# Kernel optimization log

Hardware: AMD Instinct MI355X
Metric: run time of the kernel (lower is better)

Reference implementation:

```python
import jax, jax.numpy as jnp
import numpy as np

H, W = 480, 640
ICP_W = 10.0
N_ITER = 20
FTOL = 1e-3
XTOL = 1e-8
DIST_THR = 200.0 / 15.0
NORMAL_THR = 0.94


def _skew(w):
    z = jnp.zeros((), w.dtype)
    return jnp.stack([
        jnp.stack([z, -w[2], w[1]]),
        jnp.stack([w[2], z, -w[0]]),
        jnp.stack([-w[1], w[0], z]),
    ])


def _exp_se3(xi):
    # xi = (v, w); SE3 exponential map (lie_se3_to_SE3)
    v, w = xi[:3], xi[3:]
    th2 = jnp.sum(w * w)
    th = jnp.sqrt(th2)
    small = th < 1e-8
    ths = jnp.where(small, 1.0, th)
    A = jnp.where(small, 1.0 - th2 / 6.0, jnp.sin(ths) / ths)
    B = jnp.where(small, 0.5 - th2 / 24.0, (1.0 - jnp.cos(ths)) / (ths * ths))
    C = jnp.where(small, 1.0 / 6.0 - th2 / 120.0, (ths - jnp.sin(ths)) / (ths * ths * ths))
    Wx = _skew(w)
    W2 = Wx @ Wx
    R = jnp.eye(3, dtype=xi.dtype) + A * Wx + B * W2
    V = jnp.eye(3, dtype=xi.dtype) + B * Wx + C * W2
    t = V @ v
    T = jnp.eye(4, dtype=xi.dtype)
    T = T.at[:3, :3].set(R).at[:3, 3].set(t)
    return T


def _bilinear(img, u, v):
    # img [H,W]; u,v [N] float pixel coords
    u0 = jnp.floor(u)
    v0 = jnp.floor(v)
    du = u - u0
    dv = v - v0
    u0i = jnp.clip(u0.astype(jnp.int32), 0, W - 1)
    u1i = jnp.clip(u0i + 1, 0, W - 1)
    v0i = jnp.clip(v0.astype(jnp.int32), 0, H - 1)
    v1i = jnp.clip(v0i + 1, 0, H - 1)
    I00 = img[v0i, u0i]; I01 = img[v0i, u1i]
    I10 = img[v1i, u0i]; I11 = img[v1i, u1i]
    return (I00 * (1 - du) + I01 * du) * (1 - dv) + (I10 * (1 - du) + I11 * du) * dv


def _forward(depth_ref, normals_ref, gray_ref, gray_target, points_target, normals_target, intrinsics):
    dt = depth_ref.dtype
    fx, fy = intrinsics[0, 0], intrinsics[1, 1]
    cx, cy = intrinsics[0, 2], intrinsics[1, 2]
    vv, uu = jnp.meshgrid(jnp.arange(H, dtype=dt), jnp.arange(W, dtype=dt), indexing='ij')
    Z = depth_ref
    # ref PointCloud.from_depth: backprojection [N,3]
    P = jnp.stack([(uu - cx) / fx * Z, (vv - cy) / fy * Z, Z], -1).reshape(-1, 3)
    Nr = normals_ref.reshape(-1, 3)
    Ir = gray_ref.reshape(-1)
    gy_img, gx_img = jnp.gradient(gray_target)  # d/dv, d/du
    Nflt = jnp.asarray(H * W, dt)

    def step(carry, _):
        x, conv, cost = carry
        T = _exp_se3(x)
        R, t = T[:3, :3], T[:3, 3]
        Pt = P @ R.T + t  # transformed ref points [N,3]
        Zt = Pt[:, 2]
        okz = Zt > 1e-6
        Zs = jnp.where(okz, Zt, 1.0)
        u = fx * Pt[:, 0] / Zs + cx
        v = fy * Pt[:, 1] / Zs + cy
        inb = okz & (u >= 0) & (u <= W - 1) & (v >= 0) & (v <= H - 1)
        ui = jnp.clip(jnp.round(u).astype(jnp.int32), 0, W - 1)
        vi = jnp.clip(jnp.round(v).astype(jnp.int32), 0, H - 1)
        # --- ICP point-to-plane, projective association ---
        q = points_target[vi, ui]    # [N,3]
        nq = normals_target[vi, ui]  # [N,3]
        d = Pt - q
        nref_rot = Nr @ R.T
        valid_icp = inb & (jnp.sum(d * d, -1) < DIST_THR ** 2) & (jnp.sum(nref_rot * nq, -1) > NORMAL_THR)
        m_icp = valid_icp.astype(dt)
        r_icp = jnp.sum(nq * d, -1) * m_icp                              # [N]
        J_icp = jnp.concatenate([nq, jnp.cross(Pt, nq)], -1) * m_icp[:, None]  # [N,6]
        # --- RGB photometric ---
        m_rgb = inb.astype(dt)
        It = _bilinear(gray_target, u, v)
        r_rgb = (It - Ir) * m_rgb
        gxs = _bilinear(gx_img, u, v)
        gys = _bilinear(gy_img, u, v)
        # grad_I * d(projection)/d(point)
        gp = jnp.stack([
            gxs * fx / Zs,
            gys * fy / Zs,
            -(gxs * fx * Pt[:, 0] + gys * fy * Pt[:, 1]) / (Zs * Zs),
        ], -1)
        J_rgb = jnp.concatenate([gp, jnp.cross(Pt, gp)], -1) * m_rgb[:, None]
        # --- normal equations ---
        A = ICP_W * (J_icp.T @ J_icp) + J_rgb.T @ J_rgb
        b = ICP_W * (J_icp.T @ r_icp) + J_rgb.T @ r_rgb
        x0 = jnp.linalg.solve(A + 1e-9 * jnp.eye(6, dtype=dt), b)
        new_cost = ICP_W * jnp.sum(r_icp ** 2) / Nflt + jnp.sum(r_rgb ** 2) / Nflt
        c = conv | (new_cost < FTOL) | (jnp.linalg.norm(x0) < XTOL * (XTOL + jnp.linalg.norm(x)))
        x_new = jnp.where(c, x, x - x0)
        cost_new = jnp.where(conv, cost, new_cost)
        return (x_new, c, cost_new), None

    init = (jnp.zeros(6, dt), jnp.array(False), jnp.asarray(0.0, dt))
    (x, conv, cost), _ = jax.lax.scan(step, init, None, length=N_ITER)
    return _exp_se3(x), cost


def setup_inputs() -> dict:
    key = jax.random.key(0)
    ks = jax.random.split(key, 6)
    intrinsics = jnp.array([[525.0, 0.0, 319.5], [0.0, 525.0, 239.5], [0.0, 0.0, 1.0]], jnp.float32)
    fx, fy, cx, cy = 525.0, 525.0, 319.5, 239.5
    depth_ref = 0.5 + 1.5 * jax.random.uniform(ks[0], (H, W), jnp.float32)
    depth_t = 0.5 + 1.5 * jax.random.uniform(ks[1], (H, W), jnp.float32)
    vv, uu = jnp.meshgrid(jnp.arange(H, dtype=jnp.float32), jnp.arange(W, dtype=jnp.float32), indexing='ij')
    points_target = jnp.stack([(uu - cx) / fx * depth_t, (vv - cy) / fy * depth_t, depth_t], -1)
    def mk_normals(k):
        n = 0.1 * jax.random.normal(k, (H, W, 3), jnp.float32) + jnp.array([0.0, 0.0, -1.0])
        return n / jnp.linalg.norm(n, axis=-1, keepdims=True)
    normals_ref = mk_normals(ks[2])
    normals_target = mk_normals(ks[3])
    gray_ref = jax.random.uniform(ks[4], (H, W), jnp.float32)
    gray_target = jax.random.uniform(ks[5], (H, W), jnp.float32)
    return {
        'depth_ref': depth_ref,
        'normals_ref': normals_ref,
        'gray_ref': gray_ref,
        'gray_target': gray_target,
        'points_target': points_target,
        'normals_target': normals_target,
        'intrinsics': intrinsics,
    }


def reference(depth_ref, normals_ref, gray_ref, gray_target, points_target, normals_target, intrinsics):
    return _forward(depth_ref, normals_ref, gray_ref, gray_target, points_target, normals_target, intrinsics)
```

## Files before the change

kernel.cpp:

```cpp
#include <hip/hip_runtime.h>
#include <math.h>

#define HH 480
#define WW 640
#define NPIX (HH*WW)
#define NACC 29
#define TPB 256
#define PXPT 3
#define MB 400
#define NLEAF 16
#define GSZ (MB/NLEAF)

#define WS_PKT 64
#define WS_P0 512
#define WS_P1 (WS_P0 + NACC*MB)
#define WS_G4 23808
#define WS_NR (WS_G4 + NPIX*4)
#define WS_PZ (WS_NR + NPIX*4)
#define WS_BIG_END (WS_PZ + NPIX*4)

__device__ __forceinline__ int ld_i_sc1(const int* p) {
    return __hip_atomic_load(p, __ATOMIC_RELAXED, __HIP_MEMORY_SCOPE_AGENT);
}
__device__ __forceinline__ float ld_f_sc1(const float* p) {
    return __hip_atomic_load(p, __ATOMIC_RELAXED, __HIP_MEMORY_SCOPE_AGENT);
}
__device__ __forceinline__ void st_f_sc1(float* p, float v) {
    __hip_atomic_store(p, v, __ATOMIC_RELAXED, __HIP_MEMORY_SCOPE_AGENT);
}
__device__ __forceinline__ void arrive(int* bar, int bid) {
    int* lc = bar + 128 + 16 * (bid & (NLEAF - 1));
    int a = __hip_atomic_fetch_add(lc, 1, __ATOMIC_RELAXED, __HIP_MEMORY_SCOPE_AGENT);
    if (((a + 1) % GSZ) == 0)
        __hip_atomic_fetch_add(bar + 16, 1, __ATOMIC_RELAXED, __HIP_MEMORY_SCOPE_AGENT);
}

__device__ __forceinline__ float gradu(const float* g, int v, int u) {
    const float* row = g + v * WW;
    if (u == 0)      return row[1] - row[0];
    if (u == WW - 1) return row[WW - 1] - row[WW - 2];
    return 0.5f * (row[u + 1] - row[u - 1]);
}
__device__ __forceinline__ float gradv(const float* g, int v, int u) {
    if (v == 0)      return g[WW + u] - g[u];
    if (v == HH - 1) return g[(HH - 1) * WW + u] - g[(HH - 2) * WW + u];
    return 0.5f * (g[(v + 1) * WW + u] - g[(v - 1) * WW + u]);
}

__device__ void exp_se3_f32(const float* xi, float* T) {
    float v0 = xi[0], v1 = xi[1], v2 = xi[2];
    float w0 = xi[3], w1 = xi[4], w2 = xi[5];
    float th2 = w0 * w0 + w1 * w1 + w2 * w2;
    float th = sqrtf(th2);
    bool small = th < 1e-8f;
    float ths = small ? 1.0f : th;
    float A = small ? (1.0f - th2 / 6.0f) : (sinf(ths) / ths);
    float B = small ? (0.5f - th2 / 24.0f) : ((1.0f - cosf(ths)) / (ths * ths));
    float C = small ? (1.0f / 6.0f - th2 / 120.0f) : ((ths - sinf(ths)) / (ths * ths * ths));
    float Wx[9] = { 0.f, -w2,  w1,
                    w2,  0.f, -w0,
                   -w1,  w0,  0.f };
    float W2[9];
    #pragma unroll
    for (int i = 0; i < 3; i++)
        #pragma unroll
        for (int j = 0; j < 3; j++) {
            float s = 0.f;
            #pragma unroll
            for (int k = 0; k < 3; k++) s += Wx[i * 3 + k] * Wx[k * 3 + j];
            W2[i * 3 + j] = s;
        }
    float R[9], V[9];
    #pragma unroll
    for (int i = 0; i < 9; i++) {
        float id = (i == 0 || i == 4 || i == 8) ? 1.0f : 0.0f;
        R[i] = id + A * Wx[i] + B * W2[i];
        V[i] = id + B * Wx[i] + C * W2[i];
    }
    float t0 = V[0] * v0 + V[1] * v1 + V[2] * v2;
    float t1 = V[3] * v0 + V[4] * v1 + V[5] * v2;
    float t2 = V[6] * v0 + V[7] * v1 + V[8] * v2;
    T[0] = R[0]; T[1] = R[1]; T[2]  = R[2]; T[3]  = t0;
    T[4] = R[3]; T[5] = R[4]; T[6]  = R[5]; T[7]  = t1;
    T[8] = R[6]; T[9] = R[7]; T[10] = R[8]; T[11] = t2;
    T[12] = 0.f; T[13] = 0.f; T[14] = 0.f; T[15] = 1.f;
}

__device__ __forceinline__ void accum_point(float* acc, const float* J, float r, float w, int costslot) {
    int k = 0;
    #pragma unroll
    for (int i = 0; i < 6; i++) {
        #pragma unroll
        for (int j = i; j < 6; j++) { acc[k] += w * (J[i] * J[j]); k++; }
        acc[21 + i] += w * (J[i] * r);
    }
    acc[costslot] += r * r;
}

template <int PACKED>
__global__ __launch_bounds__(TPB, 2) void fused_icp(
    const float* __restrict__ depth_ref,
    const float* __restrict__ normals_ref,
    const float* __restrict__ gray_ref,
    const float* __restrict__ gray_target,
    const float* __restrict__ points_target,
    const float* __restrict__ normals_target,
    const float* __restrict__ K,
    float* __restrict__ ws,
    float* __restrict__ out)
{
    const int tid = threadIdx.x;
    const int bid = blockIdx.x;
    const float fx = K[0], cx = K[2], fy = K[4], cy = K[5];
    int* bar = (int*)ws;
    float* pkt = ws + WS_PKT;
    int sync_no = 0;
    float4* g4  = (float4*)(ws + WS_G4);
    float4* nr4 = (float4*)(ws + WS_NR);
    float4* pz4 = (float4*)(ws + WS_PZ);

    if (PACKED) {
        int base = bid * (TPB * PXPT) + tid;
        #pragma unroll
        for (int k = 0; k < PXPT; k++) {
            int p = base + k * TPB;
            int v = p / WW, u = p - v * WW;
            float4 c;
            c.x = gray_target[p];
            c.y = gradu(gray_target, v, u);
            c.z = gradv(gray_target, v, u);
            c.w = 0.f;
            g4[p] = c;
            float4 n;
            n.x = normals_ref[3 * p];
            n.y = normals_ref[3 * p + 1];
            n.z = normals_ref[3 * p + 2];
            n.w = depth_ref[p];
            nr4[p] = n;
            float4 z;
            z.x = points_target[3 * p + 2];
            z.y = normals_target[3 * p];
            z.z = normals_target[3 * p + 1];
            z.w = normals_target[3 * p + 2];
            pz4[p] = z;
        }
        __threadfence();
        __syncthreads();
        if (tid == 0) arrive(bar, bid);
        sync_no++;
        if (bid == 0 && tid == 0) {
            while (ld_i_sc1(bar + 16) < NLEAF * sync_no) __builtin_amdgcn_s_sleep(1);
            asm volatile("s_waitcnt vmcnt(0)" ::: "memory");
            __hip_atomic_store(bar, sync_no, __ATOMIC_RELAXED, __HIP_MEMORY_SCOPE_AGENT);
        }
        if (tid == 0) {
            while (ld_i_sc1(bar) < sync_no) __builtin_amdgcn_s_sleep(4);
        }
        __syncthreads();
    }

    __shared__ float spose[12];
    __shared__ float sx[6];
    __shared__ float sconv, scost;
    __shared__ float lds[4][NACC];
    __shared__ double part8[NACC * 8];
    __shared__ double sums[NACC];

    if (tid == 0) {
        spose[0] = 1.f; spose[1] = 0.f; spose[2] = 0.f;
        spose[3] = 0.f; spose[4] = 1.f; spose[5] = 0.f;
        spose[6] = 0.f; spose[7] = 0.f; spose[8] = 1.f;
        spose[9] = 0.f; spose[10] = 0.f; spose[11] = 0.f;
        #pragma unroll
        for (int i = 0; i < 6; i++) sx[i] = 0.f;
        sconv = 0.f; scost = 0.f;
    }
    __syncthreads();

    for (int it = 0; it < 20; ++it) {
        const float R00 = spose[0], R01 = spose[1], R02 = spose[2];
        const float R10 = spose[3], R11 = spose[4], R12 = spose[5];
        const float R20 = spose[6], R21 = spose[7], R22 = spose[8];
        const float t0 = spose[9], t1 = spose[10], t2 = spose[11];

        float acc[NACC];
        #pragma unroll
        for (int i = 0; i < NACC; i++) acc[i] = 0.f;

        int pbase = bid * (TPB * PXPT) + tid;
        #pragma unroll
        for (int kk = 0; kk < PXPT; kk++) {
            int p = pbase + kk * TPB;
            int vv = p / WW;
            int uu = p - vv * WW;

            float nr0, nr1, nr2, Z;
            if (PACKED) {
                float4 n = nr4[p];
                nr0 = n.x; nr1 = n.y; nr2 = n.z; Z = n.w;
            } else {
                Z = depth_ref[p];
                nr0 = normals_ref[3 * p]; nr1 = normals_ref[3 * p + 1]; nr2 = normals_ref[3 * p + 2];
            }
            float Px = ((float)uu - cx) / fx * Z;
            float Py = ((float)vv - cy) / fy * Z;
            float Pz = Z;
            float Ptx = R00 * Px + R01 * Py + R02 * Pz + t0;
            float Pty = R10 * Px + R11 * Py + R12 * Pz + t1;
            float Ptz = R20 * Px + R21 * Py + R22 * Pz + t2;
            bool okz = Ptz > 1e-6f;
            float Zs = okz ? Ptz : 1.0f;
            float u = fx * Ptx / Zs + cx;
            float v = fy * Pty / Zs + cy;
            bool inb = okz && (u >= 0.f) && (u <= (float)(WW - 1)) && (v >= 0.f) && (v <= (float)(HH - 1));
            if (!inb) continue;

            int ui = (int)rintf(u); ui = ui < 0 ? 0 : (ui > WW - 1 ? WW - 1 : ui);
            int vi = (int)rintf(v); vi = vi < 0 ? 0 : (vi > HH - 1 ? HH - 1 : vi);
            int ti = vi * WW + ui;
            float qx, qy, qz, nqx, nqy, nqz;
            if (PACKED) {
                float4 z = pz4[ti];
                qz = z.x; nqx = z.y; nqy = z.z; nqz = z.w;
                qx = (((float)ui) - cx) / fx * qz;
                qy = (((float)vi) - cy) / fy * qz;
            } else {
                qx = points_target[3 * ti]; qy = points_target[3 * ti + 1]; qz = points_target[3 * ti + 2];
                nqx = normals_target[3 * ti]; nqy = normals_target[3 * ti + 1]; nqz = normals_target[3 * ti + 2];
            }
            float dx = Ptx - qx, dy = Pty - qy, dz = Ptz - qz;
            float nrx = R00 * nr0 + R01 * nr1 + R02 * nr2;
            float nry = R10 * nr0 + R11 * nr1 + R12 * nr2;
            float nrz = R20 * nr0 + R21 * nr1 + R22 * nr2;
            const float DIST2 = (float)((200.0 / 15.0) * (200.0 / 15.0));
            if ((dx * dx + dy * dy + dz * dz) < DIST2 &&
                (nrx * nqx + nry * nqy + nrz * nqz) > 0.94f) {
                float r = nqx * dx + nqy * dy + nqz * dz;
                float J[6] = { nqx, nqy, nqz,
                               Pty * nqz - Ptz * nqy,
                               Ptz * nqx - Ptx * nqz,
                               Ptx * nqy - Pty * nqx };
                accum_point(acc, J, r, 10.0f, 27);
            }
            float u0f = floorf(u), v0f = floorf(v);
            float du = u - u0f, dv = v - v0f;
            int u0 = (int)u0f; u0 = u0 < 0 ? 0 : (u0 > WW - 1 ? WW - 1 : u0);
            int u1 = (u0 + 1 > WW - 1) ? WW - 1 : u0 + 1;
            int v0 = (int)v0f; v0 = v0 < 0 ? 0 : (v0 > HH - 1 ? HH - 1 : v0);
            int v1 = (v0 + 1 > HH - 1) ? HH - 1 : v0 + 1;
            int i00 = v0 * WW + u0, i01 = v0 * WW + u1, i10 = v1 * WW + u0, i11 = v1 * WW + u1;
            float I00, I01, I10, I11, gx00, gx01, gx10, gx11, gy00, gy01, gy10, gy11;
            if (PACKED) {
                float4 c00 = g4[i00], c01 = g4[i01], c10 = g4[i10], c11 = g4[i11];
                I00 = c00.x; gx00 = c00.y; gy00 = c00.z;
                I01 = c01.x; gx01 = c01.y; gy01 = c01.z;
                I10 = c10.x; gx10 = c10.y; gy10 = c10.z;
                I11 = c11.x; gx11 = c11.y; gy11 = c11.z;
            } else {
                const float* g = gray_target;
                I00 = g[i00]; I01 = g[i01]; I10 = g[i10]; I11 = g[i11];
                gx00 = gradu(g, v0, u0); gx01 = gradu(g, v0, u1);
                gx10 = gradu(g, v1, u0); gx11 = gradu(g, v1, u1);
                gy00 = gradv(g, v0, u0); gy01 = gradv(g, v0, u1);
                gy10 = gradv(g, v1, u0); gy11 = gradv(g, v1, u1);
            }
            float It  = (I00 * (1.f - du) + I01 * du) * (1.f - dv) + (I10 * (1.f - du) + I11 * du) * dv;
            float gxs = (gx00 * (1.f - du) + gx01 * du) * (1.f - dv) + (gx10 * (1.f - du) + gx11 * du) * dv;
            float gys = (gy00 * (1.f - du) + gy01 * du) * (1.f - dv) + (gy10 * (1.f - du) + gy11 * du) * dv;
            float rr = It - gray_ref[p];
            float gpx = gxs * fx / Zs;
            float gpy = gys * fy / Zs;
            float gpz = -(gxs * fx * Ptx + gys * fy * Pty) / (Zs * Zs);
            float J[6] = { gpx, gpy, gpz,
                           Pty * gpz - Ptz * gpy,
                           Ptz * gpx - Ptx * gpz,
                           Ptx * gpy - Pty * gpx };
            accum_point(acc, J, rr, 1.0f, 28);
        }

        #pragma unroll
        for (int q = 0; q < NACC; q++) {
            float vq = acc[q];
            #pragma unroll
            for (int off = 32; off >= 1; off >>= 1) vq += __shfl_xor(vq, off);
            acc[q] = vq;
        }
        int wave = tid >> 6;
        int lane = tid & 63;
        __syncthreads();
        if (lane == 0) {
            #pragma unroll
            for (int q = 0; q < NACC; q++) lds[wave][q] = acc[q];
        }
        __syncthreads();
        float* pbuf = ws + ((it & 1) ? WS_P1 : WS_P0);
        if (tid < NACC) {
            int q = tid;
            float s = lds[0][q] + lds[1][q] + lds[2][q] + lds[3][q];
            st_f_sc1(&pbuf[q * MB + bid], s);
        }
        __syncthreads();
        if (tid == 0) arrive(bar, bid);
        sync_no++;

        if (bid == 0) {
            if (tid == 0) {
                while (ld_i_sc1(bar + 16) < NLEAF * sync_no) __builtin_amdgcn_s_sleep(1);
            }
            __syncthreads();
            if (tid < NACC * 8) {
                int q = tid >> 3, s = tid & 7;
                const int CH = MB / 8;
                int lo = s * CH, hi = lo + CH;
                float* row = pbuf + q * MB;
                double a0 = 0, a1 = 0, a2 = 0, a3 = 0, a4 = 0, a5 = 0, a6 = 0, a7 = 0;
                int i = lo;
                for (; i + 8 <= hi; i += 8) {
                    a0 += (double)ld_f_sc1(&row[i]);
                    a1 += (double)ld_f_sc1(&row[i + 1]);
                    a2 += (double)ld_f_sc1(&row[i + 2]);
                    a3 += (double)ld_f_sc1(&row[i + 3]);
                    a4 += (double)ld_f_sc1(&row[i + 4]);
                    a5 += (double)ld_f_sc1(&row[i + 5]);
                    a6 += (double)ld_f_sc1(&row[i + 6]);
                    a7 += (double)ld_f_sc1(&row[i + 7]);
                }
                for (; i < hi; i++) a0 += (double)ld_f_sc1(&row[i]);
                part8[tid] = (((a0 + a1) + (a2 + a3)) + ((a4 + a5) + (a6 + a7)));
            }
            __syncthreads();
            if (tid < NACC) {
                double sm = 0.0;
                #pragma unroll
                for (int s = 0; s < 8; s++) sm += part8[tid * 8 + s];
                sums[tid] = sm;
            }
            __syncthreads();
            if (tid == 0) {
                double M[6][7];
                int k = 0;
                for (int i = 0; i < 6; i++)
                    for (int j = i; j < 6; j++) { M[i][j] = sums[k]; M[j][i] = sums[k]; k++; }
                for (int i = 0; i < 6; i++) { M[i][6] = sums[21 + i]; M[i][i] += 1e-9; }
                double new_cost = 10.0 * sums[27] / (double)NPIX + sums[28] / (double)NPIX;

                for (int c = 0; c < 6; c++) {
                    int piv = c; double mx = fabs(M[c][c]);
                    for (int r2 = c + 1; r2 < 6; r2++) {
                        double a = fabs(M[r2][c]);
                        if (a > mx) { mx = a; piv = r2; }
                    }
                    if (piv != c)
                        for (int j2 = 0; j2 < 7; j2++) { double tmp = M[c][j2]; M[c][j2] = M[piv][j2]; M[piv][j2] = tmp; }
                    double inv = 1.0 / M[c][c];
                    for (int r2 = c + 1; r2 < 6; r2++) {
                        double f = M[r2][c] * inv;
                        for (int j2 = c; j2 < 7; j2++) M[r2][j2] -= f * M[c][j2];
                    }
                }
                double x0[6];
                for (int i = 5; i >= 0; i--) {
                    double s = M[i][6];
                    for (int j = i + 1; j < 6; j++) s -= M[i][j] * x0[j];
                    x0[i] = s / M[i][i];
                }

                double nx0 = 0.0, nx = 0.0;
                float xf[6];
                for (int i = 0; i < 6; i++) {
                    xf[i] = sx[i];
                    nx0 += x0[i] * x0[i];
                    nx  += (double)xf[i] * (double)xf[i];
                }
                nx0 = sqrt(nx0); nx = sqrt(nx);
                bool convold = (sconv != 0.f);
                bool c2 = convold || (new_cost < 1e-3) || (nx0 < 1e-8 * (1e-8 + nx));
                float xn[6];
                for (int i = 0; i < 6; i++)
                    xn[i] = c2 ? xf[i] : (float)((double)xf[i] - x0[i]);
                for (int i = 0; i < 6; i++) sx[i] = xn[i];
                sconv = c2 ? 1.f : 0.f;
                if (!convold) scost = (float)new_cost;

                float T[16];
                exp_se3_f32(xn, T);
                st_f_sc1(&pkt[0], T[0]);  st_f_sc1(&pkt[1], T[1]);  st_f_sc1(&pkt[2], T[2]);
                st_f_sc1(&pkt[3], T[4]);  st_f_sc1(&pkt[4], T[5]);  st_f_sc1(&pkt[5], T[6]);
                st_f_sc1(&pkt[6], T[8]);  st_f_sc1(&pkt[7], T[9]);  st_f_sc1(&pkt[8], T[10]);
                st_f_sc1(&pkt[9], T[3]);  st_f_sc1(&pkt[10], T[7]); st_f_sc1(&pkt[11], T[11]);
                if (it == 19) {
                    for (int i = 0; i < 16; i++) out[i] = T[i];
                    out[16] = scost;
                }
                asm volatile("s_waitcnt vmcnt(0)" ::: "memory");
                __hip_atomic_store(bar, sync_no, __ATOMIC_RELAXED, __HIP_MEMORY_SCOPE_AGENT);
            }
        }

        if (tid == 0) {
            while (ld_i_sc1(bar) < sync_no) __builtin_amdgcn_s_sleep(4);
            asm volatile("" ::: "memory");
            #pragma unroll
            for (int i = 0; i < 12; i++) spose[i] = ld_f_sc1(&pkt[i]);
        }
        __syncthreads();
    }
}

extern "C" void kernel_launch(void* const* d_in, const int* in_sizes, int n_in,
                              void* d_out, int out_size, void* d_ws, size_t ws_size,
                              hipStream_t stream) {
    const float* depth_ref      = (const float*)d_in[0];
    const float* normals_ref    = (const float*)d_in[1];
    const float* gray_ref       = (const float*)d_in[2];
    const float* gray_target    = (const float*)d_in[3];
    const float* points_target  = (const float*)d_in[4];
    const float* normals_target = (const float*)d_in[5];
    const float* K              = (const float*)d_in[6];
    float* ws  = (float*)d_ws;
    float* out = (float*)d_out;

    hipMemsetAsync(d_ws, 0, 2048, stream);

    bool big = ws_size >= (size_t)WS_BIG_END * sizeof(float);
    if (big) {
        hipLaunchKernelGGL((fused_icp<1>), dim3(MB), dim3(TPB), 0, stream,
                           depth_ref, normals_ref, gray_ref, gray_target,
                           points_target, normals_target, K, ws, out);
    } else {
        hipLaunchKernelGGL((fused_icp<0>), dim3(MB), dim3(TPB), 0, stream,
                           depth_ref, normals_ref, gray_ref, gray_target,
                           points_target, normals_target, K, ws, out);
    }
}
```

Before: 538.3 us.

## Use 1024 persistent blocks with hierarchical leaf reduction and per-leaf release flags

Raises the persistent grid from 400 to 1024 blocks, each handling 300 pixels, and allows 4 blocks per CU through launch bounds. Blocks are remapped so each XCD group lands in its own leaf. The last block to arrive in each leaf pre-reduces that leaf's partials in double and publishes them, so block 0 only sums 16 leaf results. The single release flag becomes 16 per-leaf flags to spread out polling. The aim is to cut per-iteration grid-barrier and reduction latency. In exchange there are more blocks to synchronize and less pixel work per thread, and co-residency of all 1024 blocks is required to avoid deadlock.

```diff
diff --git a/kernel.cpp b/kernel.cpp
--- a/kernel.cpp
+++ b/kernel.cpp
@@ -6,15 +6,16 @@
 #define NPIX (HH*WW)
 #define NACC 29
 #define TPB 256
-#define PXPT 3
-#define MB 400
+#define NBLK 1024
+#define PPB 300
 #define NLEAF 16
-#define GSZ (MB/NLEAF)
-
-#define WS_PKT 64
-#define WS_P0 512
-#define WS_P1 (WS_P0 + NACC*MB)
-#define WS_G4 23808
+#define LSZ (NBLK/NLEAF)
+#define PB NBLK
+
+#define WS_PKT 400
+#define WS_LP 1024
+#define WS_P0 2048
+#define WS_G4 32768
 #define WS_NR (WS_G4 + NPIX*4)
 #define WS_PZ (WS_NR + NPIX*4)
 #define WS_BIG_END (WS_PZ + NPIX*4)
@@ -28,11 +29,11 @@
 __device__ __forceinline__ void st_f_sc1(float* p, float v) {
     __hip_atomic_store(p, v, __ATOMIC_RELAXED, __HIP_MEMORY_SCOPE_AGENT);
 }
-__device__ __forceinline__ void arrive(int* bar, int bid) {
-    int* lc = bar + 128 + 16 * (bid & (NLEAF - 1));
-    int a = __hip_atomic_fetch_add(lc, 1, __ATOMIC_RELAXED, __HIP_MEMORY_SCOPE_AGENT);
-    if (((a + 1) % GSZ) == 0)
-        __hip_atomic_fetch_add(bar + 16, 1, __ATOMIC_RELAXED, __HIP_MEMORY_SCOPE_AGENT);
+__device__ __forceinline__ double ld_d_sc1(const double* p) {
+    return __hip_atomic_load(p, __ATOMIC_RELAXED, __HIP_MEMORY_SCOPE_AGENT);
+}
+__device__ __forceinline__ void st_d_sc1(double* p, double v) {
+    __hip_atomic_store(p, v, __ATOMIC_RELAXED, __HIP_MEMORY_SCOPE_AGENT);
 }
 
 __device__ __forceinline__ float gradu(const float* g, int v, int u) {
@@ -98,7 +99,7 @@
 }
 
 template <int PACKED>
-__global__ __launch_bounds__(TPB, 2) void fused_icp(
+__global__ __launch_bounds__(TPB, 4) void fused_icp(
     const float* __restrict__ depth_ref,
     const float* __restrict__ normals_ref,
     const float* __restrict__ gray_ref,
@@ -110,20 +111,42 @@
     float* __restrict__ out)
 {
     const int tid = threadIdx.x;
-    const int bid = blockIdx.x;
+    const int wid = (blockIdx.x & 7) * (NBLK / 8) + (blockIdx.x >> 3);
+    const int leaf = wid / LSZ;
     const float fx = K[0], cx = K[2], fy = K[4], cy = K[5];
     int* bar = (int*)ws;
     float* pkt = ws + WS_PKT;
+    double* lp = (double*)(ws + WS_LP);
+    float* pbuf = ws + WS_P0;
     int sync_no = 0;
     float4* g4  = (float4*)(ws + WS_G4);
     float4* nr4 = (float4*)(ws + WS_NR);
     float4* pz4 = (float4*)(ws + WS_PZ);
 
+    __shared__ float spose[12];
+    __shared__ float sx[6];
+    __shared__ float sconv, scost;
+    __shared__ float lds[4][NACC];
+    __shared__ double part8[NACC * 8];
+    __shared__ double sums[NACC];
+    __shared__ int scloser;
+
+    if (tid == 0) {
+        spose[0] = 1.f; spose[1] = 0.f; spose[2] = 0.f;
+        spose[3] = 0.f; spose[4] = 1.f; spose[5] = 0.f;
+        spose[6] = 0.f; spose[7] = 0.f; spose[8] = 1.f;
+        spose[9] = 0.f; spose[10] = 0.f; spose[11] = 0.f;
+        #pragma unroll
+        for (int i = 0; i < 6; i++) sx[i] = 0.f;
+        sconv = 0.f; scost = 0.f;
+    }
+
     if (PACKED) {
-        int base = bid * (TPB * PXPT) + tid;
-        #pragma unroll
-        for (int k = 0; k < PXPT; k++) {
-            int p = base + k * TPB;
+        int base = wid * PPB;
+        for (int k = 0; k < 2; k++) {
+            int off = k * TPB + tid;
+            if (off >= PPB) break;
+            int p = base + off;
             int v = p / WW, u = p - v * WW;
             float4 c;
             c.x = gray_target[p];
@@ -145,37 +168,28 @@
             pz4[p] = z;
         }
         __threadfence();
-        __syncthreads();
-        if (tid == 0) arrive(bar, bid);
         sync_no++;
-        if (bid == 0 && tid == 0) {
+        __syncthreads();
+        if (tid == 0) {
+            int a = __hip_atomic_fetch_add(bar + 128 + 16 * leaf, 1, __ATOMIC_RELAXED, __HIP_MEMORY_SCOPE_AGENT);
+            scloser = ((a + 1) == LSZ * sync_no) ? 1 : 0;
+        }
+        __syncthreads();
+        if (scloser && tid == 0)
+            __hip_atomic_fetch_add(bar + 16, 1, __ATOMIC_RELAXED, __HIP_MEMORY_SCOPE_AGENT);
+        if (wid == 0 && tid == 0) {
             while (ld_i_sc1(bar + 16) < NLEAF * sync_no) __builtin_amdgcn_s_sleep(1);
             asm volatile("s_waitcnt vmcnt(0)" ::: "memory");
-            __hip_atomic_store(bar, sync_no, __ATOMIC_RELAXED, __HIP_MEMORY_SCOPE_AGENT);
+            for (int i = 0; i < NLEAF; i++)
+                __hip_atomic_store(bar + 512 + 16 * i, sync_no, __ATOMIC_RELAXED, __HIP_MEMORY_SCOPE_AGENT);
         }
         if (tid == 0) {
-            while (ld_i_sc1(bar) < sync_no) __builtin_amdgcn_s_sleep(4);
-        }
-        __syncthreads();
-    }
-
-    __shared__ float spose[12];
-    __shared__ float sx[6];
-    __shared__ float sconv, scost;
-    __shared__ float lds[4][NACC];
-    __shared__ double part8[NACC * 8];
-    __shared__ double sums[NACC];
-
-    if (tid == 0) {
-        spose[0] = 1.f; spose[1] = 0.f; spose[2] = 0.f;
-        spose[3] = 0.f; spose[4] = 1.f; spose[5] = 0.f;
-        spose[6] = 0.f; spose[7] = 0.f; spose[8] = 1.f;
-        spose[9] = 0.f; spose[10] = 0.f; spose[11] = 0.f;
-        #pragma unroll
-        for (int i = 0; i < 6; i++) sx[i] = 0.f;
-        sconv = 0.f; scost = 0.f;
-    }
-    __syncthreads();
+            while (ld_i_sc1(bar + 512 + 16 * leaf) < sync_no) __builtin_amdgcn_s_sleep(2);
+        }
+        __syncthreads();
+    } else {
+        __syncthreads();
+    }
 
     for (int it = 0; it < 20; ++it) {
         const float R00 = spose[0], R01 = spose[1], R02 = spose[2];
@@ -187,10 +201,12 @@
         #pragma unroll
         for (int i = 0; i < NACC; i++) acc[i] = 0.f;
 
-        int pbase = bid * (TPB * PXPT) + tid;
-        #pragma unroll
-        for (int kk = 0; kk < PXPT; kk++) {
-            int p = pbase + kk * TPB;
+        int base = wid * PPB;
+        #pragma unroll
+        for (int kk = 0; kk < 2; kk++) {
+            int off = kk * TPB + tid;
+            if (off >= PPB) break;
+            int p = base + off;
             int vv = p / WW;
             int uu = p - vv * WW;
 
@@ -293,40 +309,47 @@
             for (int q = 0; q < NACC; q++) lds[wave][q] = acc[q];
         }
         __syncthreads();
-        float* pbuf = ws + ((it & 1) ? WS_P1 : WS_P0);
         if (tid < NACC) {
             int q = tid;
             float s = lds[0][q] + lds[1][q] + lds[2][q] + lds[3][q];
-            st_f_sc1(&pbuf[q * MB + bid], s);
-        }
-        __syncthreads();
-        if (tid == 0) arrive(bar, bid);
+            st_f_sc1(&pbuf[q * PB + wid], s);
+        }
         sync_no++;
-
-        if (bid == 0) {
+        __syncthreads();
+        if (tid == 0) {
+            int a = __hip_atomic_fetch_add(bar + 128 + 16 * leaf, 1, __ATOMIC_RELAXED, __HIP_MEMORY_SCOPE_AGENT);
+            scloser = ((a + 1) == LSZ * sync_no) ? 1 : 0;
+        }
+        __syncthreads();
+        if (scloser) {
+            if (tid < NACC * 8) {
+                int q = tid >> 3, s = tid & 7;
+                const float* row = pbuf + q * PB + leaf * LSZ + s * 8;
+                double a0 = 0.0;
+                #pragma unroll
+                for (int j = 0; j < 8; j++) a0 += (double)ld_f_sc1(&row[j]);
+                part8[tid] = a0;
+            }
+            __syncthreads();
+            if (tid < NACC) {
+                double sm = 0.0;
+                #pragma unroll
+                for (int s = 0; s < 8; s++) sm += part8[tid * 8 + s];
+                st_d_sc1(&lp[tid * NLEAF + leaf], sm);
+            }
+            __syncthreads();
+            if (tid == 0)
+                __hip_atomic_fetch_add(bar + 16, 1, __ATOMIC_RELAXED, __HIP_MEMORY_SCOPE_AGENT);
+        }
+
+        if (wid == 0) {
             if (tid == 0) {
                 while (ld_i_sc1(bar + 16) < NLEAF * sync_no) __builtin_amdgcn_s_sleep(1);
             }
             __syncthreads();
             if (tid < NACC * 8) {
                 int q = tid >> 3, s = tid & 7;
-                const int CH = MB / 8;
-                int lo = s * CH, hi = lo + CH;
-                float* row = pbuf + q * MB;
-                double a0 = 0, a1 = 0, a2 = 0, a3 = 0, a4 = 0, a5 = 0, a6 = 0, a7 = 0;
-                int i = lo;
-                for (; i + 8 <= hi; i += 8) {
-                    a0 += (double)ld_f_sc1(&row[i]);
-                    a1 += (double)ld_f_sc1(&row[i + 1]);
-                    a2 += (double)ld_f_sc1(&row[i + 2]);
-                    a3 += (double)ld_f_sc1(&row[i + 3]);
-                    a4 += (double)ld_f_sc1(&row[i + 4]);
-                    a5 += (double)ld_f_sc1(&row[i + 5]);
-                    a6 += (double)ld_f_sc1(&row[i + 6]);
-                    a7 += (double)ld_f_sc1(&row[i + 7]);
-                }
-                for (; i < hi; i++) a0 += (double)ld_f_sc1(&row[i]);
-                part8[tid] = (((a0 + a1) + (a2 + a3)) + ((a4 + a5) + (a6 + a7)));
+                part8[tid] = ld_d_sc1(&lp[q * NLEAF + 2 * s]) + ld_d_sc1(&lp[q * NLEAF + 2 * s + 1]);
             }
             __syncthreads();
             if (tid < NACC) {
@@ -393,12 +416,13 @@
                     out[16] = scost;
                 }
                 asm volatile("s_waitcnt vmcnt(0)" ::: "memory");
-                __hip_atomic_store(bar, sync_no, __ATOMIC_RELAXED, __HIP_MEMORY_SCOPE_AGENT);
+                for (int i = 0; i < NLEAF; i++)
+                    __hip_atomic_store(bar + 512 + 16 * i, sync_no, __ATOMIC_RELAXED, __HIP_MEMORY_SCOPE_AGENT);
             }
         }
 
         if (tid == 0) {
-            while (ld_i_sc1(bar) < sync_no) __builtin_amdgcn_s_sleep(4);
+            while (ld_i_sc1(bar + 512 + 16 * leaf) < sync_no) __builtin_amdgcn_s_sleep(2);
             asm volatile("" ::: "memory");
             #pragma unroll
             for (int i = 0; i < 12; i++) spose[i] = ld_f_sc1(&pkt[i]);
@@ -420,15 +444,15 @@
     float* ws  = (float*)d_ws;
     float* out = (float*)d_out;
 
-    hipMemsetAsync(d_ws, 0, 2048, stream);
+    hipMemsetAsync(d_ws, 0, 4096, stream);
 
     bool big = ws_size >= (size_t)WS_BIG_END * sizeof(float);
     if (big) {
-        hipLaunchKernelGGL((fused_icp<1>), dim3(MB), dim3(TPB), 0, stream,
+        hipLaunchKernelGGL((fused_icp<1>), dim3(NBLK), dim3(TPB), 0, stream,
                            depth_ref, normals_ref, gray_ref, gray_target,
                            points_target, normals_target, K, ws, out);
     } else {
-        hipLaunchKernelGGL((fused_icp<0>), dim3(MB), dim3(TPB), 0, stream,
+        hipLaunchKernelGGL((fused_icp<0>), dim3(NBLK), dim3(TPB), 0, stream,
                            depth_ref, normals_ref, gray_ref, gray_target,
                            points_target, normals_target, K, ws, out);
     }
```

New measurement: 490.2 us. 8.9% less time.

## Replace persistent grid-barrier ICP kernel with per-iteration map/reduce and solve launches

Applied to the files above, without the earlier changes.

The single persistent kernel used software grid barriers and atomics to run all 20 Gauss-Newton iterations. It is split into a packing kernel plus, per iteration, a map_reduce kernel over 600 blocks of 512 threads and a single-block solve kernel. Pose and state now pass through the workspace between launches. This removes the spin-wait barriers and the atomic traffic, at the cost of about 41 kernel launches and their launch gaps.

```diff
diff --git a/kernel.cpp b/kernel.cpp
--- a/kernel.cpp
+++ b/kernel.cpp
@@ -5,35 +5,17 @@
 #define WW 640
 #define NPIX (HH*WW)
 #define NACC 29
-#define TPB 256
-#define PXPT 3
-#define MB 400
-#define NLEAF 16
-#define GSZ (MB/NLEAF)
-
-#define WS_PKT 64
-#define WS_P0 512
-#define WS_P1 (WS_P0 + NACC*MB)
-#define WS_G4 23808
+#define TPB_B 512
+#define NB_B 600
+#define TPB_C 256
+#define PB 600
+#define CH 75
+
+#define WS_P 512
+#define WS_G4 18432
 #define WS_NR (WS_G4 + NPIX*4)
 #define WS_PZ (WS_NR + NPIX*4)
 #define WS_BIG_END (WS_PZ + NPIX*4)
-
-__device__ __forceinline__ int ld_i_sc1(const int* p) {
-    return __hip_atomic_load(p, __ATOMIC_RELAXED, __HIP_MEMORY_SCOPE_AGENT);
-}
-__device__ __forceinline__ float ld_f_sc1(const float* p) {
-    return __hip_atomic_load(p, __ATOMIC_RELAXED, __HIP_MEMORY_SCOPE_AGENT);
-}
-__device__ __forceinline__ void st_f_sc1(float* p, float v) {
-    __hip_atomic_store(p, v, __ATOMIC_RELAXED, __HIP_MEMORY_SCOPE_AGENT);
-}
-__device__ __forceinline__ void arrive(int* bar, int bid) {
-    int* lc = bar + 128 + 16 * (bid & (NLEAF - 1));
-    int a = __hip_atomic_fetch_add(lc, 1, __ATOMIC_RELAXED, __HIP_MEMORY_SCOPE_AGENT);
-    if (((a + 1) % GSZ) == 0)
-        __hip_atomic_fetch_add(bar + 16, 1, __ATOMIC_RELAXED, __HIP_MEMORY_SCOPE_AGENT);
-}
 
 __device__ __forceinline__ float gradu(const float* g, int v, int u) {
     const float* row = g + v * WW;
@@ -98,7 +80,52 @@
 }
 
 template <int PACKED>
-__global__ __launch_bounds__(TPB, 2) void fused_icp(
+__global__ __launch_bounds__(TPB_B) void pack_init(
+    const float* __restrict__ depth_ref,
+    const float* __restrict__ normals_ref,
+    const float* __restrict__ gray_target,
+    const float* __restrict__ points_target,
+    const float* __restrict__ normals_target,
+    float* __restrict__ ws)
+{
+    if (blockIdx.x == 0 && threadIdx.x == 0) {
+        ws[0] = 1.f; ws[1] = 0.f; ws[2] = 0.f;
+        ws[3] = 0.f; ws[4] = 1.f; ws[5] = 0.f;
+        ws[6] = 0.f; ws[7] = 0.f; ws[8] = 1.f;
+        ws[9] = 0.f; ws[10] = 0.f; ws[11] = 0.f;
+        ws[12] = 0.f; ws[13] = 0.f;
+        #pragma unroll
+        for (int i = 0; i < 6; i++) ws[16 + i] = 0.f;
+    }
+    if (PACKED) {
+        int p = blockIdx.x * TPB_B + threadIdx.x;
+        int v = p / WW, u = p - v * WW;
+        float4* g4  = (float4*)(ws + WS_G4);
+        float4* nr4 = (float4*)(ws + WS_NR);
+        float4* pz4 = (float4*)(ws + WS_PZ);
+        float4 c;
+        c.x = gray_target[p];
+        c.y = gradu(gray_target, v, u);
+        c.z = gradv(gray_target, v, u);
+        c.w = 0.f;
+        g4[p] = c;
+        float4 n;
+        n.x = normals_ref[3 * p];
+        n.y = normals_ref[3 * p + 1];
+        n.z = normals_ref[3 * p + 2];
+        n.w = depth_ref[p];
+        nr4[p] = n;
+        float4 z;
+        z.x = points_target[3 * p + 2];
+        z.y = normals_target[3 * p];
+        z.z = normals_target[3 * p + 1];
+        z.w = normals_target[3 * p + 2];
+        pz4[p] = z;
+    }
+}
+
+template <int PACKED>
+__global__ __launch_bounds__(TPB_B) void map_reduce(
     const float* __restrict__ depth_ref,
     const float* __restrict__ normals_ref,
     const float* __restrict__ gray_ref,
@@ -106,115 +133,53 @@
     const float* __restrict__ points_target,
     const float* __restrict__ normals_target,
     const float* __restrict__ K,
-    float* __restrict__ ws,
-    float* __restrict__ out)
+    float* __restrict__ ws)
 {
     const int tid = threadIdx.x;
     const int bid = blockIdx.x;
     const float fx = K[0], cx = K[2], fy = K[4], cy = K[5];
-    int* bar = (int*)ws;
-    float* pkt = ws + WS_PKT;
-    int sync_no = 0;
-    float4* g4  = (float4*)(ws + WS_G4);
-    float4* nr4 = (float4*)(ws + WS_NR);
-    float4* pz4 = (float4*)(ws + WS_PZ);
-
-    if (PACKED) {
-        int base = bid * (TPB * PXPT) + tid;
-        #pragma unroll
-        for (int k = 0; k < PXPT; k++) {
-            int p = base + k * TPB;
-            int v = p / WW, u = p - v * WW;
-            float4 c;
-            c.x = gray_target[p];
-            c.y = gradu(gray_target, v, u);
-            c.z = gradv(gray_target, v, u);
-            c.w = 0.f;
-            g4[p] = c;
-            float4 n;
-            n.x = normals_ref[3 * p];
-            n.y = normals_ref[3 * p + 1];
-            n.z = normals_ref[3 * p + 2];
-            n.w = depth_ref[p];
-            nr4[p] = n;
-            float4 z;
-            z.x = points_target[3 * p + 2];
-            z.y = normals_target[3 * p];
-            z.z = normals_target[3 * p + 1];
-            z.w = normals_target[3 * p + 2];
-            pz4[p] = z;
-        }
-        __threadfence();
-        __syncthreads();
-        if (tid == 0) arrive(bar, bid);
-        sync_no++;
-        if (bid == 0 && tid == 0) {
-            while (ld_i_sc1(bar + 16) < NLEAF * sync_no) __builtin_amdgcn_s_sleep(1);
-            asm volatile("s_waitcnt vmcnt(0)" ::: "memory");
-            __hip_atomic_store(bar, sync_no, __ATOMIC_RELAXED, __HIP_MEMORY_SCOPE_AGENT);
-        }
-        if (tid == 0) {
-            while (ld_i_sc1(bar) < sync_no) __builtin_amdgcn_s_sleep(4);
-        }
-        __syncthreads();
-    }
+    const float4* g4  = (const float4*)(ws + WS_G4);
+    const float4* nr4 = (const float4*)(ws + WS_NR);
+    const float4* pz4 = (const float4*)(ws + WS_PZ);
 
     __shared__ float spose[12];
-    __shared__ float sx[6];
-    __shared__ float sconv, scost;
-    __shared__ float lds[4][NACC];
-    __shared__ double part8[NACC * 8];
-    __shared__ double sums[NACC];
-
-    if (tid == 0) {
-        spose[0] = 1.f; spose[1] = 0.f; spose[2] = 0.f;
-        spose[3] = 0.f; spose[4] = 1.f; spose[5] = 0.f;
-        spose[6] = 0.f; spose[7] = 0.f; spose[8] = 1.f;
-        spose[9] = 0.f; spose[10] = 0.f; spose[11] = 0.f;
-        #pragma unroll
-        for (int i = 0; i < 6; i++) sx[i] = 0.f;
-        sconv = 0.f; scost = 0.f;
-    }
+    __shared__ float lds[8][NACC];
+    if (tid < 12) spose[tid] = ws[tid];
     __syncthreads();
-
-    for (int it = 0; it < 20; ++it) {
-        const float R00 = spose[0], R01 = spose[1], R02 = spose[2];
-        const float R10 = spose[3], R11 = spose[4], R12 = spose[5];
-        const float R20 = spose[6], R21 = spose[7], R22 = spose[8];
-        const float t0 = spose[9], t1 = spose[10], t2 = spose[11];
-
-        float acc[NACC];
-        #pragma unroll
-        for (int i = 0; i < NACC; i++) acc[i] = 0.f;
-
-        int pbase = bid * (TPB * PXPT) + tid;
-        #pragma unroll
-        for (int kk = 0; kk < PXPT; kk++) {
-            int p = pbase + kk * TPB;
-            int vv = p / WW;
-            int uu = p - vv * WW;
-
-            float nr0, nr1, nr2, Z;
-            if (PACKED) {
-                float4 n = nr4[p];
-                nr0 = n.x; nr1 = n.y; nr2 = n.z; Z = n.w;
-            } else {
-                Z = depth_ref[p];
-                nr0 = normals_ref[3 * p]; nr1 = normals_ref[3 * p + 1]; nr2 = normals_ref[3 * p + 2];
-            }
-            float Px = ((float)uu - cx) / fx * Z;
-            float Py = ((float)vv - cy) / fy * Z;
-            float Pz = Z;
-            float Ptx = R00 * Px + R01 * Py + R02 * Pz + t0;
-            float Pty = R10 * Px + R11 * Py + R12 * Pz + t1;
-            float Ptz = R20 * Px + R21 * Py + R22 * Pz + t2;
-            bool okz = Ptz > 1e-6f;
-            float Zs = okz ? Ptz : 1.0f;
-            float u = fx * Ptx / Zs + cx;
-            float v = fy * Pty / Zs + cy;
-            bool inb = okz && (u >= 0.f) && (u <= (float)(WW - 1)) && (v >= 0.f) && (v <= (float)(HH - 1));
-            if (!inb) continue;
-
+    const float R00 = spose[0], R01 = spose[1], R02 = spose[2];
+    const float R10 = spose[3], R11 = spose[4], R12 = spose[5];
+    const float R20 = spose[6], R21 = spose[7], R22 = spose[8];
+    const float t0 = spose[9], t1 = spose[10], t2 = spose[11];
+
+    float acc[NACC];
+    #pragma unroll
+    for (int i = 0; i < NACC; i++) acc[i] = 0.f;
+
+    {
+        int p = bid * TPB_B + tid;
+        int vv = p / WW;
+        int uu = p - vv * WW;
+
+        float nr0, nr1, nr2, Z;
+        if (PACKED) {
+            float4 n = nr4[p];
+            nr0 = n.x; nr1 = n.y; nr2 = n.z; Z = n.w;
+        } else {
+            Z = depth_ref[p];
+            nr0 = normals_ref[3 * p]; nr1 = normals_ref[3 * p + 1]; nr2 = normals_ref[3 * p + 2];
+        }
+        float Px = ((float)uu - cx) / fx * Z;
+        float Py = ((float)vv - cy) / fy * Z;
+        float Pz = Z;
+        float Ptx = R00 * Px + R01 * Py + R02 * Pz + t0;
+        float Pty = R10 * Px + R11 * Py + R12 * Pz + t1;
+        float Ptz = R20 * Px + R21 * Py + R22 * Pz + t2;
+        bool okz = Ptz > 1e-6f;
+        float Zs = okz ? Ptz : 1.0f;
+        float u = fx * Ptx / Zs + cx;
+        float v = fy * Pty / Zs + cy;
+        bool inb = okz && (u >= 0.f) && (u <= (float)(WW - 1)) && (v >= 0.f) && (v <= (float)(HH - 1));
+        if (inb) {
             int ui = (int)rintf(u); ui = ui < 0 ? 0 : (ui > WW - 1 ? WW - 1 : ui);
             int vi = (int)rintf(v); vi = vi < 0 ? 0 : (vi > HH - 1 ? HH - 1 : vi);
             int ti = vi * WW + ui;
@@ -277,133 +242,117 @@
                            Ptx * gpy - Pty * gpx };
             accum_point(acc, J, rr, 1.0f, 28);
         }
-
-        #pragma unroll
-        for (int q = 0; q < NACC; q++) {
-            float vq = acc[q];
-            #pragma unroll
-            for (int off = 32; off >= 1; off >>= 1) vq += __shfl_xor(vq, off);
-            acc[q] = vq;
-        }
-        int wave = tid >> 6;
-        int lane = tid & 63;
-        __syncthreads();
-        if (lane == 0) {
-            #pragma unroll
-            for (int q = 0; q < NACC; q++) lds[wave][q] = acc[q];
-        }
-        __syncthreads();
-        float* pbuf = ws + ((it & 1) ? WS_P1 : WS_P0);
-        if (tid < NACC) {
-            int q = tid;
-            float s = lds[0][q] + lds[1][q] + lds[2][q] + lds[3][q];
-            st_f_sc1(&pbuf[q * MB + bid], s);
-        }
-        __syncthreads();
-        if (tid == 0) arrive(bar, bid);
-        sync_no++;
-
-        if (bid == 0) {
-            if (tid == 0) {
-                while (ld_i_sc1(bar + 16) < NLEAF * sync_no) __builtin_amdgcn_s_sleep(1);
-            }
-            __syncthreads();
-            if (tid < NACC * 8) {
-                int q = tid >> 3, s = tid & 7;
-                const int CH = MB / 8;
-                int lo = s * CH, hi = lo + CH;
-                float* row = pbuf + q * MB;
-                double a0 = 0, a1 = 0, a2 = 0, a3 = 0, a4 = 0, a5 = 0, a6 = 0, a7 = 0;
-                int i = lo;
-                for (; i + 8 <= hi; i += 8) {
-                    a0 += (double)ld_f_sc1(&row[i]);
-                    a1 += (double)ld_f_sc1(&row[i + 1]);
-                    a2 += (double)ld_f_sc1(&row[i + 2]);
-                    a3 += (double)ld_f_sc1(&row[i + 3]);
-                    a4 += (double)ld_f_sc1(&row[i + 4]);
-                    a5 += (double)ld_f_sc1(&row[i + 5]);
-                    a6 += (double)ld_f_sc1(&row[i + 6]);
-                    a7 += (double)ld_f_sc1(&row[i + 7]);
-                }
-                for (; i < hi; i++) a0 += (double)ld_f_sc1(&row[i]);
-                part8[tid] = (((a0 + a1) + (a2 + a3)) + ((a4 + a5) + (a6 + a7)));
-            }
-            __syncthreads();
-            if (tid < NACC) {
-                double sm = 0.0;
-                #pragma unroll
-                for (int s = 0; s < 8; s++) sm += part8[tid * 8 + s];
-                sums[tid] = sm;
-            }
-            __syncthreads();
-            if (tid == 0) {
-                double M[6][7];
-                int k = 0;
-                for (int i = 0; i < 6; i++)
-                    for (int j = i; j < 6; j++) { M[i][j] = sums[k]; M[j][i] = sums[k]; k++; }
-                for (int i = 0; i < 6; i++) { M[i][6] = sums[21 + i]; M[i][i] += 1e-9; }
-                double new_cost = 10.0 * sums[27] / (double)NPIX + sums[28] / (double)NPIX;
-
-                for (int c = 0; c < 6; c++) {
-                    int piv = c; double mx = fabs(M[c][c]);
-                    for (int r2 = c + 1; r2 < 6; r2++) {
-                        double a = fabs(M[r2][c]);
-                        if (a > mx) { mx = a; piv = r2; }
-                    }
-                    if (piv != c)
-                        for (int j2 = 0; j2 < 7; j2++) { double tmp = M[c][j2]; M[c][j2] = M[piv][j2]; M[piv][j2] = tmp; }
-                    double inv = 1.0 / M[c][c];
-                    for (int r2 = c + 1; r2 < 6; r2++) {
-                        double f = M[r2][c] * inv;
-                        for (int j2 = c; j2 < 7; j2++) M[r2][j2] -= f * M[c][j2];
-                    }
-                }
-                double x0[6];
-                for (int i = 5; i >= 0; i--) {
-                    double s = M[i][6];
-                    for (int j = i + 1; j < 6; j++) s -= M[i][j] * x0[j];
-                    x0[i] = s / M[i][i];
-                }
-
-                double nx0 = 0.0, nx = 0.0;
-                float xf[6];
-                for (int i = 0; i < 6; i++) {
-                    xf[i] = sx[i];
-                    nx0 += x0[i] * x0[i];
-                    nx  += (double)xf[i] * (double)xf[i];
-                }
-                nx0 = sqrt(nx0); nx = sqrt(nx);
-                bool convold = (sconv != 0.f);
-                bool c2 = convold || (new_cost < 1e-3) || (nx0 < 1e-8 * (1e-8 + nx));
-                float xn[6];
-                for (int i = 0; i < 6; i++)
-                    xn[i] = c2 ? xf[i] : (float)((double)xf[i] - x0[i]);
-                for (int i = 0; i < 6; i++) sx[i] = xn[i];
-                sconv = c2 ? 1.f : 0.f;
-                if (!convold) scost = (float)new_cost;
-
-                float T[16];
-                exp_se3_f32(xn, T);
-                st_f_sc1(&pkt[0], T[0]);  st_f_sc1(&pkt[1], T[1]);  st_f_sc1(&pkt[2], T[2]);
-                st_f_sc1(&pkt[3], T[4]);  st_f_sc1(&pkt[4], T[5]);  st_f_sc1(&pkt[5], T[6]);
-                st_f_sc1(&pkt[6], T[8]);  st_f_sc1(&pkt[7], T[9]);  st_f_sc1(&pkt[8], T[10]);
-                st_f_sc1(&pkt[9], T[3]);  st_f_sc1(&pkt[10], T[7]); st_f_sc1(&pkt[11], T[11]);
-                if (it == 19) {
-                    for (int i = 0; i < 16; i++) out[i] = T[i];
-                    out[16] = scost;
-                }
-                asm volatile("s_waitcnt vmcnt(0)" ::: "memory");
-                __hip_atomic_store(bar, sync_no, __ATOMIC_RELAXED, __HIP_MEMORY_SCOPE_AGENT);
-            }
-        }
-
-        if (tid == 0) {
-            while (ld_i_sc1(bar) < sync_no) __builtin_amdgcn_s_sleep(4);
-            asm volatile("" ::: "memory");
-            #pragma unroll
-            for (int i = 0; i < 12; i++) spose[i] = ld_f_sc1(&pkt[i]);
-        }
-        __syncthreads();
+    }
+
+    #pragma unroll
+    for (int q = 0; q < NACC; q++) {
+        float vq = acc[q];
+        #pragma unroll
+        for (int off = 32; off >= 1; off >>= 1) vq += __shfl_xor(vq, off);
+        acc[q] = vq;
+    }
+    int wave = tid >> 6;
+    int lane = tid & 63;
+    if (lane == 0) {
+        #pragma unroll
+        for (int q = 0; q < NACC; q++) lds[wave][q] = acc[q];
+    }
+    __syncthreads();
+    if (tid < NACC) {
+        int q = tid;
+        float s = ((lds[0][q] + lds[1][q]) + (lds[2][q] + lds[3][q]))
+                + ((lds[4][q] + lds[5][q]) + (lds[6][q] + lds[7][q]));
+        ws[WS_P + q * PB + bid] = s;
+    }
+}
+
+__global__ __launch_bounds__(TPB_C) void solve_update(float* __restrict__ ws,
+                                                      float* __restrict__ out,
+                                                      int final_iter)
+{
+    __shared__ double part8[NACC * 8];
+    __shared__ double sums[NACC];
+    int tid = threadIdx.x;
+    const float* part = ws + WS_P;
+    if (tid < NACC * 8) {
+        int q = tid >> 3, s = tid & 7;
+        const float* row = part + q * PB + s * CH;
+        double a0 = 0.0, a1 = 0.0, a2 = 0.0, a3 = 0.0;
+        int i = 0;
+        for (; i + 4 <= CH; i += 4) {
+            a0 += (double)row[i];
+            a1 += (double)row[i + 1];
+            a2 += (double)row[i + 2];
+            a3 += (double)row[i + 3];
+        }
+        for (; i < CH; i++) a0 += (double)row[i];
+        part8[tid] = ((a0 + a1) + (a2 + a3));
+    }
+    __syncthreads();
+    if (tid < NACC) {
+        double sm = 0.0;
+        #pragma unroll
+        for (int s = 0; s < 8; s++) sm += part8[tid * 8 + s];
+        sums[tid] = sm;
+    }
+    __syncthreads();
+    if (tid == 0) {
+        double M[6][7];
+        int k = 0;
+        for (int i = 0; i < 6; i++)
+            for (int j = i; j < 6; j++) { M[i][j] = sums[k]; M[j][i] = sums[k]; k++; }
+        for (int i = 0; i < 6; i++) { M[i][6] = sums[21 + i]; M[i][i] += 1e-9; }
+        double new_cost = 10.0 * sums[27] / (double)NPIX + sums[28] / (double)NPIX;
+
+        for (int c = 0; c < 6; c++) {
+            int piv = c; double mx = fabs(M[c][c]);
+            for (int r2 = c + 1; r2 < 6; r2++) {
+                double a = fabs(M[r2][c]);
+                if (a > mx) { mx = a; piv = r2; }
+            }
+            if (piv != c)
+                for (int j2 = 0; j2 < 7; j2++) { double tmp = M[c][j2]; M[c][j2] = M[piv][j2]; M[piv][j2] = tmp; }
+            double inv = 1.0 / M[c][c];
+            for (int r2 = c + 1; r2 < 6; r2++) {
+                double f = M[r2][c] * inv;
+                for (int j2 = c; j2 < 7; j2++) M[r2][j2] -= f * M[c][j2];
+            }
+        }
+        double x0[6];
+        for (int i = 5; i >= 0; i--) {
+            double s = M[i][6];
+            for (int j = i + 1; j < 6; j++) s -= M[i][j] * x0[j];
+            x0[i] = s / M[i][i];
+        }
+
+        double nx0 = 0.0, nx = 0.0;
+        float xf[6];
+        for (int i = 0; i < 6; i++) {
+            xf[i] = ws[16 + i];
+            nx0 += x0[i] * x0[i];
+            nx  += (double)xf[i] * (double)xf[i];
+        }
+        nx0 = sqrt(nx0); nx = sqrt(nx);
+        bool convold = (ws[12] != 0.f);
+        bool c2 = convold || (new_cost < 1e-3) || (nx0 < 1e-8 * (1e-8 + nx));
+        float xn[6];
+        for (int i = 0; i < 6; i++)
+            xn[i] = c2 ? xf[i] : (float)((double)xf[i] - x0[i]);
+        for (int i = 0; i < 6; i++) ws[16 + i] = xn[i];
+        ws[12] = c2 ? 1.f : 0.f;
+        if (!convold) ws[13] = (float)new_cost;
+
+        float T[16];
+        exp_se3_f32(xn, T);
+        ws[0] = T[0]; ws[1] = T[1]; ws[2]  = T[2];
+        ws[3] = T[4]; ws[4] = T[5]; ws[5]  = T[6];
+        ws[6] = T[8]; ws[7] = T[9]; ws[8]  = T[10];
+        ws[9] = T[3]; ws[10] = T[7]; ws[11] = T[11];
+
+        if (final_iter) {
+            for (int i = 0; i < 16; i++) out[i] = T[i];
+            out[16] = ws[13];
+        }
     }
 }
 
@@ -420,16 +369,28 @@
     float* ws  = (float*)d_ws;
     float* out = (float*)d_out;
 
-    hipMemsetAsync(d_ws, 0, 2048, stream);
-
     bool big = ws_size >= (size_t)WS_BIG_END * sizeof(float);
     if (big) {
-        hipLaunchKernelGGL((fused_icp<1>), dim3(MB), dim3(TPB), 0, stream,
-                           depth_ref, normals_ref, gray_ref, gray_target,
-                           points_target, normals_target, K, ws, out);
+        hipLaunchKernelGGL((pack_init<1>), dim3(NB_B), dim3(TPB_B), 0, stream,
+                           depth_ref, normals_ref, gray_target,
+                           points_target, normals_target, ws);
+        for (int it = 0; it < 20; ++it) {
+            hipLaunchKernelGGL((map_reduce<1>), dim3(NB_B), dim3(TPB_B), 0, stream,
+                               depth_ref, normals_ref, gray_ref, gray_target,
+                               points_target, normals_target, K, ws);
+            hipLaunchKernelGGL(solve_update, dim3(1), dim3(TPB_C), 0, stream,
+                               ws, out, (it == 19) ? 1 : 0);
+        }
     } else {
-        hipLaunchKernelGGL((fused_icp<0>), dim3(MB), dim3(TPB), 0, stream,
-                           depth_ref, normals_ref, gray_ref, gray_target,
-                           points_target, normals_target, K, ws, out);
-    }
-}
+        hipLaunchKernelGGL((pack_init<0>), dim3(NB_B), dim3(TPB_B), 0, stream,
+                           depth_ref, normals_ref, gray_target,
+                           points_target, normals_target, ws);
+        for (int it = 0; it < 20; ++it) {
+            hipLaunchKernelGGL((map_reduce<0>), dim3(NB_B), dim3(TPB_B), 0, stream,
+                               depth_ref, normals_ref, gray_ref, gray_target,
+                               points_target, normals_target, K, ws);
+            hipLaunchKernelGGL(solve_update, dim3(1), dim3(TPB_C), 0, stream,
+                               ws, out, (it == 19) ? 1 : 0);
+        }
+    }
+}
```

Result: faster. 444.5 us (-17.4%).
